# Optimization experiments

Measured on AMD Instinct MI355X. Metric: run time of the kernel, lower is better.

Reference implementation:

```python
import jax, jax.numpy as jnp
import numpy as np

NEG_SLOPE = 0.01  # torch F.leaky_relu default used in the DGL GAT-style layer


def grat_layer(h, src, dst, W, a, n_nodes):
    """One GRAT (GAT-style) layer.
    h: [N, d_in], src/dst: [E] int, W: [d_in, d_out], a: [2*d_out] (attn_fc weight
    on concat [z_src || z_dst]). Returns [N, d_out].
    """
    d_out = W.shape[1]
    z = h @ W                                   # [N, d_out]
    # attention logits per edge: a^T [z_src || z_dst]
    s_src = z @ a[:d_out]                       # [N]
    s_dst = z @ a[d_out:]                       # [N]
    e = jax.nn.leaky_relu(s_src[src] + s_dst[dst], NEG_SLOPE)  # [E]
    # numerically stable softmax over incoming edges of each dst node
    m = jax.ops.segment_max(e, dst, num_segments=n_nodes)      # [N]
    m = jnp.where(jnp.isfinite(m), m, 0.0)      # nodes with no in-edges
    w = jnp.exp(e - m[dst])                     # [E]
    denom = jax.ops.segment_sum(w, dst, num_segments=n_nodes)  # [N]
    alpha = w / jnp.maximum(denom, 1e-9)[dst]   # [E]
    # weighted scatter-aggregate of source features into dst
    out = jax.ops.segment_sum(alpha[:, None] * z[src], dst, num_segments=n_nodes)
    return out                                  # [N, d_out]


def setup_inputs() -> dict:
    key = jax.random.key(0)
    ks = jax.random.split(key, 10)
    N, E = 100000, 1600000
    IN, H1, H2, OUT = 128, 32, 32, 1
    feature = jax.random.normal(ks[0], (N, IN), dtype=jnp.float32)
    src = jax.random.randint(ks[1], (E,), 0, N, dtype=jnp.int32)
    dst = jax.random.randint(ks[2], (E,), 0, N, dtype=jnp.int32)
    s = 0.1
    W1 = jax.random.normal(ks[3], (IN, H1), dtype=jnp.float32) * s
    a1 = jax.random.normal(ks[4], (2 * H1,), dtype=jnp.float32) * s
    W2 = jax.random.normal(ks[5], (H1, H2), dtype=jnp.float32) * s
    a2 = jax.random.normal(ks[6], (2 * H2,), dtype=jnp.float32) * s
    W3 = jax.random.normal(ks[7], (H2, OUT), dtype=jnp.float32) * s
    a3 = jax.random.normal(ks[8], (2 * OUT,), dtype=jnp.float32) * s
    return {"feature": feature, "src": src, "dst": dst,
            "W1": W1, "a1": a1, "W2": W2, "a2": a2, "W3": W3, "a3": a3}


def reference(feature, src, dst, W1, a1, W2, a2, W3, a3):
    n = feature.shape[0]
    h = jax.nn.relu(grat_layer(feature, src, dst, W1, a1, n))
    h = jax.nn.relu(grat_layer(h, src, dst, W2, a2, n))
    h = grat_layer(h, src, dst, W3, a3, n)
    return jax.nn.sigmoid(h)                    # [N, 1]
```

## Files before the change

kernel.cpp:

```cpp
#include <hip/hip_runtime.h>
#include <cstdint>
#include <cstddef>

#define NEG_SLOPE 0.01f


__global__ __launch_bounds__(128) void gemm1_kernel(
    const float* __restrict__ h, const float* __restrict__ W,
    const float* __restrict__ a, float* __restrict__ z,
    float* __restrict__ s_src, float* __restrict__ s_dst, int N)
{
    __shared__ float Wl[128 * 32];
    int tid = threadIdx.x;
    int rowBase = blockIdx.x * 64;

    {
        const float4* W4 = (const float4*)W;
        float4* Wl4 = (float4*)Wl;
        for (int i = tid; i < 1024; i += 128) Wl4[i] = W4[i];
    }
    __syncthreads();

    int wv   = tid >> 6;
    int lane = tid & 63;
    int g    = lane >> 3;
    int l8   = lane & 7;
    int r0   = wv * 32 + g * 4;
    int col4 = l8 * 4;

    float acc[4][4];
#pragma unroll
    for (int i = 0; i < 4; i++)
#pragma unroll
        for (int c = 0; c < 4; c++) acc[i][c] = 0.f;

    const float4* h4  = (const float4*)h;
    const float4* Wl4 = (const float4*)Wl;

    size_t rowOff[4];
#pragma unroll
    for (int i = 0; i < 4; i++) {
        int r = rowBase + r0 + i;
        rowOff[i] = (size_t)((r < N) ? r : (N - 1)) * 32;
    }

#pragma unroll 2
    for (int kq = 0; kq < 32; kq++) {
        float4 w0 = Wl4[(kq * 4 + 0) * 8 + l8];
        float4 w1 = Wl4[(kq * 4 + 1) * 8 + l8];
        float4 w2 = Wl4[(kq * 4 + 2) * 8 + l8];
        float4 w3 = Wl4[(kq * 4 + 3) * 8 + l8];
#pragma unroll
        for (int i = 0; i < 4; i++) {
            float4 hv = h4[rowOff[i] + kq];
            acc[i][0] += hv.x * w0.x; acc[i][1] += hv.x * w0.y;
            acc[i][2] += hv.x * w0.z; acc[i][3] += hv.x * w0.w;
            acc[i][0] += hv.y * w1.x; acc[i][1] += hv.y * w1.y;
            acc[i][2] += hv.y * w1.z; acc[i][3] += hv.y * w1.w;
            acc[i][0] += hv.z * w2.x; acc[i][1] += hv.z * w2.y;
            acc[i][2] += hv.z * w2.z; acc[i][3] += hv.z * w2.w;
            acc[i][0] += hv.w * w3.x; acc[i][1] += hv.w * w3.y;
            acc[i][2] += hv.w * w3.z; acc[i][3] += hv.w * w3.w;
        }
    }

    float4 alo = ((const float4*)a)[l8];
    float4 ahi = ((const float4*)a)[8 + l8];
#pragma unroll
    for (int i = 0; i < 4; i++) {
        int row = rowBase + r0 + i;
        if (row < N) {
            float4 zv = make_float4(acc[i][0], acc[i][1], acc[i][2], acc[i][3]);
            *(float4*)&z[(size_t)row * 32 + col4] = zv;
            float ps = zv.x * alo.x + zv.y * alo.y + zv.z * alo.z + zv.w * alo.w;
            float pd = zv.x * ahi.x + zv.y * ahi.y + zv.z * ahi.z + zv.w * ahi.w;
            ps += __shfl_xor(ps, 1, 64); ps += __shfl_xor(ps, 2, 64); ps += __shfl_xor(ps, 4, 64);
            pd += __shfl_xor(pd, 1, 64); pd += __shfl_xor(pd, 2, 64); pd += __shfl_xor(pd, 4, 64);
            if (l8 == 0) { s_src[row] = ps; s_dst[row] = pd; }
        }
    }
}

__global__ __launch_bounds__(128) void gemm2_kernel(
    const float* __restrict__ h, const float* __restrict__ W,
    const float* __restrict__ a, float* __restrict__ z,
    float* __restrict__ s_src, float* __restrict__ s_dst, int N)
{
    __shared__ float Hl[64 * 44];
    __shared__ float Wl[32 * 32];
    int tid = threadIdx.x;
    int rowBase = blockIdx.x * 64;

    {
        const float4* W4 = (const float4*)W;
        float4* Wl4 = (float4*)Wl;
        for (int i = tid; i < 256; i += 128) Wl4[i] = W4[i];
    }
    {
        const float4* h4 = (const float4*)h;
        for (int i = tid; i < 64 * 8; i += 128) {
            int r = i >> 3, kq = i & 7;
            float4 v = (rowBase + r < N) ? h4[(size_t)(rowBase + r) * 8 + kq]
                                         : make_float4(0.f, 0.f, 0.f, 0.f);
            *(float4*)&Hl[r * 44 + kq * 4] = v;
        }
    }
    __syncthreads();

    int wv   = tid >> 6;
    int lane = tid & 63;
    int g    = lane >> 3;
    int l8   = lane & 7;
    int r0   = wv * 32 + g * 4;
    int col4 = l8 * 4;

    float acc[4][4];
#pragma unroll
    for (int i = 0; i < 4; i++)
#pragma unroll
        for (int c = 0; c < 4; c++) acc[i][c] = 0.f;

    const float4* H4  = (const float4*)Hl;
    const float4* Wl4 = (const float4*)Wl;

#pragma unroll
    for (int kq = 0; kq < 8; kq++) {
        float4 w0 = Wl4[(kq * 4 + 0) * 8 + l8];
        float4 w1 = Wl4[(kq * 4 + 1) * 8 + l8];
        float4 w2 = Wl4[(kq * 4 + 2) * 8 + l8];
        float4 w3 = Wl4[(kq * 4 + 3) * 8 + l8];
#pragma unroll
        for (int i = 0; i < 4; i++) {
            float4 hv = H4[(r0 + i) * 11 + kq];
            acc[i][0] += hv.x * w0.x; acc[i][1] += hv.x * w0.y;
            acc[i][2] += hv.x * w0.z; acc[i][3] += hv.x * w0.w;
            acc[i][0] += hv.y * w1.x; acc[i][1] += hv.y * w1.y;
            acc[i][2] += hv.y * w1.z; acc[i][3] += hv.y * w1.w;
            acc[i][0] += hv.z * w2.x; acc[i][1] += hv.z * w2.y;
            acc[i][2] += hv.z * w2.z; acc[i][3] += hv.z * w2.w;
            acc[i][0] += hv.w * w3.x; acc[i][1] += hv.w * w3.y;
            acc[i][2] += hv.w * w3.z; acc[i][3] += hv.w * w3.w;
        }
    }

    float4 alo = ((const float4*)a)[l8];
    float4 ahi = ((const float4*)a)[8 + l8];
#pragma unroll
    for (int i = 0; i < 4; i++) {
        int row = rowBase + r0 + i;
        if (row < N) {
            float4 zv = make_float4(acc[i][0], acc[i][1], acc[i][2], acc[i][3]);
            *(float4*)&z[(size_t)row * 32 + col4] = zv;
            float ps = zv.x * alo.x + zv.y * alo.y + zv.z * alo.z + zv.w * alo.w;
            float pd = zv.x * ahi.x + zv.y * ahi.y + zv.z * ahi.z + zv.w * ahi.w;
            ps += __shfl_xor(ps, 1, 64); ps += __shfl_xor(ps, 2, 64); ps += __shfl_xor(ps, 4, 64);
            pd += __shfl_xor(pd, 1, 64); pd += __shfl_xor(pd, 2, 64); pd += __shfl_xor(pd, 4, 64);
            if (l8 == 0) { s_src[row] = ps; s_dst[row] = pd; }
        }
    }
}

__global__ __launch_bounds__(256) void gemm3_kernel(
    const float* __restrict__ h, const float* __restrict__ W,
    const float* __restrict__ a, float2* __restrict__ zs,
    float* __restrict__ s_dst, int N)
{
    int i = blockIdx.x * 256 + threadIdx.x;
    if (i >= N) return;
    const float4* hp = (const float4*)(h + (size_t)i * 32);
    const float4* wp = (const float4*)W;
    float acc = 0.f;
#pragma unroll
    for (int c = 0; c < 8; c++) {
        float4 v = hp[c];
        float4 w = wp[c];
        acc += v.x * w.x + v.y * w.y + v.z * w.z + v.w * w.w;
    }
    zs[i] = make_float2(acc, acc * a[0]);
    s_dst[i] = acc * a[1];
}


#define TILE_E 4096
#define NB_MAX 512

__global__ __launch_bounds__(256) void csr_hist_kernel(
    const int* __restrict__ dst, int* __restrict__ counts,
    int E, int TB, int NB)
{
    __shared__ int hist[NB_MAX];
    int tid = threadIdx.x;
    int t = blockIdx.x;
    for (int b = tid; b < NB; b += 256) hist[b] = 0;
    __syncthreads();
    int base = t * TILE_E;
    for (int i = tid; i < TILE_E; i += 256) {
        int k = base + i;
        if (k < E) atomicAdd(&hist[dst[k] >> 8], 1);
    }
    __syncthreads();
    for (int b = tid; b < NB; b += 256) counts[b * TB + t] = hist[b];
}

__global__ __launch_bounds__(256) void scan1_kernel(
    const int* __restrict__ vals, int* __restrict__ incl,
    int* __restrict__ blockSums, int M)
{
    __shared__ int tmp[256];
    int tid = threadIdx.x;
    int i = blockIdx.x * 256 + tid;
    int v = (i < M) ? vals[i] : 0;
    tmp[tid] = v;
    __syncthreads();
#pragma unroll
    for (int off = 1; off < 256; off <<= 1) {
        int t = (tid >= off) ? tmp[tid - off] : 0;
        __syncthreads();
        tmp[tid] += t;
        __syncthreads();
    }
    if (i < M) incl[i] = tmp[tid];
    if (tid == 255) blockSums[blockIdx.x] = tmp[255];
}

__global__ __launch_bounds__(1024) void scan2_kernel(int* __restrict__ blockSums, int nb)
{
    __shared__ int tmp[1024];
    int tid = threadIdx.x;
    int v = (tid < nb) ? blockSums[tid] : 0;
    tmp[tid] = v;
    __syncthreads();
#pragma unroll
    for (int off = 1; off < 1024; off <<= 1) {
        int t = (tid >= off) ? tmp[tid - off] : 0;
        __syncthreads();
        tmp[tid] += t;
        __syncthreads();
    }
    if (tid < nb) blockSums[tid] = tmp[tid] - v;
}

__global__ __launch_bounds__(256) void scan3_kernel(
    const int* __restrict__ vals, const int* __restrict__ blockSums,
    int* __restrict__ cscan, int M, int E)
{
    int i = blockIdx.x * 256 + threadIdx.x;
    if (i < M) {
        cscan[i] = cscan[i] - vals[i] + blockSums[i >> 8];
    }
    if (i == 0) cscan[M] = E;
}

__global__ __launch_bounds__(256) void csr_scatter_kernel(
    const int* __restrict__ src, const int* __restrict__ dst,
    const int* __restrict__ cscan, int2* __restrict__ ebuf,
    int E, int TB, int NB)
{
    __shared__ int baseB[NB_MAX];
    __shared__ int cur[NB_MAX];
    int tid = threadIdx.x;
    int t = blockIdx.x;
    for (int b = tid; b < NB; b += 256) {
        baseB[b] = cscan[b * TB + t];
        cur[b] = 0;
    }
    __syncthreads();
    int base = t * TILE_E;
    for (int i = tid; i < TILE_E; i += 256) {
        int k = base + i;
        if (k < E) {
            int d = dst[k], s = src[k];
            int b = d >> 8;
            int r = atomicAdd(&cur[b], 1);
            ebuf[baseB[b] + r] = make_int2(s, d & 255);
        }
    }
}

__global__ __launch_bounds__(256) void csr_bucket_kernel(
    const int2* __restrict__ ebuf, const int* __restrict__ cscan,
    int* __restrict__ csr_src, int* __restrict__ offsets,
    int N, int E, int TB)
{
    __shared__ int2 eb[6144];
    __shared__ int hist[256];
    __shared__ int loff[256];
    __shared__ int tmp[256];
    int tid = threadIdx.x;
    int b = blockIdx.x;

    int beg = cscan[b * TB];
    int endv = cscan[(b + 1) * TB];
    int cnt = endv - beg;
    int first = b << 8;

    hist[tid] = 0;
    __syncthreads();

    bool inLds = (cnt <= 6144);
    for (int i = tid; i < cnt; i += 256) {
        int2 v = ebuf[beg + i];
        if (inLds) eb[i] = v;
        atomicAdd(&hist[v.y], 1);
    }
    __syncthreads();

    int hv = hist[tid];
    tmp[tid] = hv;
    __syncthreads();
#pragma unroll
    for (int off = 1; off < 256; off <<= 1) {
        int t = (tid >= off) ? tmp[tid - off] : 0;
        __syncthreads();
        tmp[tid] += t;
        __syncthreads();
    }
    loff[tid] = tmp[tid] - hv;
    __syncthreads();

    if (first + tid < N) offsets[first + tid] = beg + loff[tid];
    if (b == 0 && tid == 0) offsets[N] = E;

    hist[tid] = 0;
    __syncthreads();

    for (int i = tid; i < cnt; i += 256) {
        int2 v = inLds ? eb[i] : ebuf[beg + i];
        int r = atomicAdd(&hist[v.y], 1);
        csr_src[beg + loff[v.y] + r] = v.x;
    }
}


__global__ __launch_bounds__(256) void agg32_fused_kernel(
    const int* __restrict__ offsets, const int* __restrict__ csr_src,
    const float* __restrict__ s_src, const float* __restrict__ s_dst,
    const float* __restrict__ z, float* __restrict__ h, int N)
{
    __shared__ float2 wsbuf[8 * 128];
    int g    = threadIdx.x >> 5;
    int lane = threadIdx.x & 31;
    int node = blockIdx.x * 8 + g;
    if (node >= N) return;
    float2* ws = &wsbuf[g * 128];

    int beg = offsets[node], end = offsets[node + 1];
    int deg = end - beg;
    float sd = s_dst[node];
    float o = 0.f;
    float rden;

    if (deg <= 128) {
        int   sreg[4];
        float ev[4];
        int nIter = (deg + 31) >> 5;
        float m = -3.0e38f;
#pragma unroll 4
        for (int it = 0; it < nIter; ++it) {
            int p = beg + it * 32 + lane;
            float e = -3.0e38f;
            int s = 0;
            if (p < end) {
                s = csr_src[p];
                e = s_src[s] + sd;
                e = (e > 0.f) ? e : NEG_SLOPE * e;
            }
            sreg[it] = s;
            ev[it] = e;
            m = fmaxf(m, e);
        }
#pragma unroll
        for (int off = 16; off > 0; off >>= 1) m = fmaxf(m, __shfl_xor(m, off, 32));

        float l = 0.f;
#pragma unroll 4
        for (int it = 0; it < nIter; ++it) {
            int p = beg + it * 32 + lane;
            float w = (p < end) ? __expf(ev[it] - m) : 0.f;
            ws[it * 32 + lane] = make_float2(w, __int_as_float(sreg[it]));
            l += w;
        }
#pragma unroll
        for (int off = 16; off > 0; off >>= 1) l += __shfl_xor(l, off, 32);
        rden = 1.f / fmaxf(l, 1e-9f);

        int p = 0;
        for (; p + 4 <= deg; p += 4) {
            float2 a0 = ws[p],     a1 = ws[p + 1];
            float2 a2 = ws[p + 2], a3 = ws[p + 3];
            int s0 = __float_as_int(a0.y), s1 = __float_as_int(a1.y);
            int s2 = __float_as_int(a2.y), s3 = __float_as_int(a3.y);
            float z0 = z[(size_t)s0 * 32 + lane];
            float z1 = z[(size_t)s1 * 32 + lane];
            float z2 = z[(size_t)s2 * 32 + lane];
            float z3 = z[(size_t)s3 * 32 + lane];
            o += a0.x * z0;
            o += a1.x * z1;
            o += a2.x * z2;
            o += a3.x * z3;
        }
        for (; p < deg; ++p) {
            float2 aa = ws[p];
            o += aa.x * z[(size_t)__float_as_int(aa.y) * 32 + lane];
        }
    } else {
        float m = -3.0e38f;
        for (int p = beg + lane; p < end; p += 32) {
            float e = s_src[csr_src[p]] + sd;
            e = (e > 0.f) ? e : NEG_SLOPE * e;
            m = fmaxf(m, e);
        }
#pragma unroll
        for (int off = 16; off > 0; off >>= 1) m = fmaxf(m, __shfl_xor(m, off, 32));
        float l = 0.f;
        for (int p = beg + lane; p < end; p += 32) {
            float e = s_src[csr_src[p]] + sd;
            e = (e > 0.f) ? e : NEG_SLOPE * e;
            l += __expf(e - m);
        }
#pragma unroll
        for (int off = 16; off > 0; off >>= 1) l += __shfl_xor(l, off, 32);
        rden = 1.f / fmaxf(l, 1e-9f);
        for (int p = beg; p < end; ++p) {
            int s = csr_src[p];
            float e = s_src[s] + sd;
            e = (e > 0.f) ? e : NEG_SLOPE * e;
            float w = __expf(e - m);
            o += w * z[(size_t)s * 32 + lane];
        }
    }

    float v = o * rden;
    h[(size_t)node * 32 + lane] = (v > 0.f) ? v : 0.f;
}

__global__ __launch_bounds__(256) void agg1_fused_kernel(
    const int* __restrict__ offsets, const int* __restrict__ csr_src,
    const float2* __restrict__ zs, const float* __restrict__ s_dst,
    float* __restrict__ out, int N)
{
    int node = blockIdx.x * 8 + (threadIdx.x >> 5);
    int lane = threadIdx.x & 31;
    if (node >= N) return;

    int beg = offsets[node], end = offsets[node + 1];
    int deg = end - beg;
    float sd = s_dst[node];

    if (deg <= 128) {
        float ev[4], zv[4];
        int nIter = (deg + 31) >> 5;
        float m = -3.0e38f;
#pragma unroll 4
        for (int it = 0; it < nIter; ++it) {
            int p = beg + it * 32 + lane;
            float e = -3.0e38f, zz = 0.f;
            if (p < end) {
                float2 v2 = zs[csr_src[p]];
                zz = v2.x;
                e = v2.y + sd;
                e = (e > 0.f) ? e : NEG_SLOPE * e;
            }
            ev[it] = e; zv[it] = zz;
            m = fmaxf(m, e);
        }
#pragma unroll
        for (int off = 16; off > 0; off >>= 1) m = fmaxf(m, __shfl_xor(m, off, 32));
        float l = 0.f, o = 0.f;
#pragma unroll 4
        for (int it = 0; it < nIter; ++it) {
            int p = beg + it * 32 + lane;
            float w = (p < end) ? __expf(ev[it] - m) : 0.f;
            l += w;
            o += w * zv[it];
        }
#pragma unroll
        for (int off = 16; off > 0; off >>= 1) {
            l += __shfl_xor(l, off, 32);
            o += __shfl_xor(o, off, 32);
        }
        if (lane == 0) {
            float v = o / fmaxf(l, 1e-9f);
            out[node] = 1.f / (1.f + __expf(-v));
        }
    } else {
        float m = -3.0e38f;
        for (int p = beg + lane; p < end; p += 32) {
            float e = zs[csr_src[p]].y + sd;
            e = (e > 0.f) ? e : NEG_SLOPE * e;
            m = fmaxf(m, e);
        }
#pragma unroll
        for (int off = 16; off > 0; off >>= 1) m = fmaxf(m, __shfl_xor(m, off, 32));
        float l = 0.f, o = 0.f;
        for (int p = beg + lane; p < end; p += 32) {
            float2 v2 = zs[csr_src[p]];
            float e = v2.y + sd;
            e = (e > 0.f) ? e : NEG_SLOPE * e;
            float w = __expf(e - m);
            l += w; o += w * v2.x;
        }
#pragma unroll
        for (int off = 16; off > 0; off >>= 1) {
            l += __shfl_xor(l, off, 32);
            o += __shfl_xor(o, off, 32);
        }
        if (lane == 0) {
            float v = o / fmaxf(l, 1e-9f);
            out[node] = 1.f / (1.f + __expf(-v));
        }
    }
}


extern "C" void kernel_launch(void* const* d_in, const int* in_sizes, int n_in,
                              void* d_out, int out_size, void* d_ws, size_t ws_size,
                              hipStream_t stream)
{
    const float* feature = (const float*)d_in[0];
    const int*   src     = (const int*)d_in[1];
    const int*   dst     = (const int*)d_in[2];
    const float* W1      = (const float*)d_in[3];
    const float* a1      = (const float*)d_in[4];
    const float* W2      = (const float*)d_in[5];
    const float* a2      = (const float*)d_in[6];
    const float* W3      = (const float*)d_in[7];
    const float* a3      = (const float*)d_in[8];
    float* out = (float*)d_out;

    const int N = in_sizes[0] / 128;
    const int E = in_sizes[1];

    const int TB = (E + TILE_E - 1) / TILE_E;
    const int NB = (N + 255) >> 8;
    const int M  = NB * TB;

    char* p = (char*)d_ws;
    float* zbuf    = (float*)p;  p += (size_t)N * 32 * sizeof(float);
    float* hbuf    = (float*)p;  p += (size_t)N * 32 * sizeof(float);
    float* s_src   = (float*)p;  p += (size_t)N * sizeof(float);
    float* s_dst   = (float*)p;  p += (size_t)N * sizeof(float);
    int*   offsets = (int*)p;    p += ((size_t)N + 1) * sizeof(int);
    int*   counts  = (int*)p;    p += ((size_t)M + 1) * sizeof(int);
    int*   cscan   = (int*)p;    p += ((size_t)M + 1) * sizeof(int);
    int*   blockSums = (int*)p;  p += 1024 * sizeof(int);
    int2*  ebuf    = (int2*)p;   p += (size_t)E * sizeof(int2);
    int*   csr_src = (int*)p;    p += (size_t)E * sizeof(int);

    const int nodeBlocks8  = (N + 7) / 8;
    const int nodeBlocks   = (N + 255) / 256;
    const int gemmBlocks64 = (N + 63) / 64;
    const int scanBlocksM  = (M + 255) / 256;

    hipLaunchKernelGGL(csr_hist_kernel, dim3(TB), dim3(256), 0, stream,
                       dst, counts, E, TB, NB);
    hipLaunchKernelGGL(scan1_kernel, dim3(scanBlocksM), dim3(256), 0, stream,
                       counts, cscan, blockSums, M);
    hipLaunchKernelGGL(scan2_kernel, dim3(1), dim3(1024), 0, stream,
                       blockSums, scanBlocksM);
    hipLaunchKernelGGL(scan3_kernel, dim3(scanBlocksM), dim3(256), 0, stream,
                       counts, blockSums, cscan, M, E);
    hipLaunchKernelGGL(csr_scatter_kernel, dim3(TB), dim3(256), 0, stream,
                       src, dst, cscan, ebuf, E, TB, NB);
    hipLaunchKernelGGL(csr_bucket_kernel, dim3(NB), dim3(256), 0, stream,
                       ebuf, cscan, csr_src, offsets, N, E, TB);

    hipLaunchKernelGGL(gemm1_kernel, dim3(gemmBlocks64), dim3(128), 0, stream,
                       feature, W1, a1, zbuf, s_src, s_dst, N);
    hipLaunchKernelGGL(agg32_fused_kernel, dim3(nodeBlocks8), dim3(256), 0, stream,
                       offsets, csr_src, s_src, s_dst, zbuf, hbuf, N);

    hipLaunchKernelGGL(gemm2_kernel, dim3(gemmBlocks64), dim3(128), 0, stream,
                       hbuf, W2, a2, zbuf, s_src, s_dst, N);
    hipLaunchKernelGGL(agg32_fused_kernel, dim3(nodeBlocks8), dim3(256), 0, stream,
                       offsets, csr_src, s_src, s_dst, zbuf, hbuf, N);

    float2* zs = (float2*)zbuf;
    hipLaunchKernelGGL(gemm3_kernel, dim3(nodeBlocks), dim3(256), 0, stream,
                       hbuf, W3, a3, zs, s_dst, N);
    hipLaunchKernelGGL(agg1_fused_kernel, dim3(nodeBlocks8), dim3(256), 0, stream,
                       offsets, csr_src, zs, s_dst, out, N);
}
```

Before: 280.7 us.

## Store intermediate features in bf16 and pack CSR edge buffer into single ints

The two hidden-layer GEMMs now write z as bf16 instead of fp32, and the aggregation kernels gather and convert bf16 rows. This halves the bytes of the random per-edge feature gathers. Attention scores are still computed from the fp32 accumulators. Separately, the CSR build packs source and local destination into one 32-bit int, which halves the edge buffer traffic and lets more buckets fit in LDS. Risks are precision loss in the aggregated features and the packing only being valid for source ids below 2^23.

```diff
diff --git a/kernel.cpp b/kernel.cpp
--- a/kernel.cpp
+++ b/kernel.cpp
@@ -1,13 +1,23 @@
 #include <hip/hip_runtime.h>
+#include <hip/hip_bf16.h>
 #include <cstdint>
 #include <cstddef>
 
 #define NEG_SLOPE 0.01f
 
+static __device__ __forceinline__ unsigned short f2bf(float f) {
+    __hip_bfloat16 b = __float2bfloat16(f);
+    return *(unsigned short*)&b;
+}
+static __device__ __forceinline__ float bf2f(unsigned short u) {
+    __hip_bfloat16 b = *(__hip_bfloat16*)&u;
+    return __bfloat162float(b);
+}
+
 
 __global__ __launch_bounds__(128) void gemm1_kernel(
     const float* __restrict__ h, const float* __restrict__ W,
-    const float* __restrict__ a, float* __restrict__ z,
+    const float* __restrict__ a, unsigned short* __restrict__ zb,
     float* __restrict__ s_src, float* __restrict__ s_dst, int N)
 {
     __shared__ float Wl[128 * 32];
@@ -70,10 +80,11 @@
     for (int i = 0; i < 4; i++) {
         int row = rowBase + r0 + i;
         if (row < N) {
-            float4 zv = make_float4(acc[i][0], acc[i][1], acc[i][2], acc[i][3]);
-            *(float4*)&z[(size_t)row * 32 + col4] = zv;
-            float ps = zv.x * alo.x + zv.y * alo.y + zv.z * alo.z + zv.w * alo.w;
-            float pd = zv.x * ahi.x + zv.y * ahi.y + zv.z * ahi.z + zv.w * ahi.w;
+            ushort4 zv4 = make_ushort4(f2bf(acc[i][0]), f2bf(acc[i][1]),
+                                       f2bf(acc[i][2]), f2bf(acc[i][3]));
+            *(ushort4*)&zb[(size_t)row * 32 + col4] = zv4;
+            float ps = acc[i][0] * alo.x + acc[i][1] * alo.y + acc[i][2] * alo.z + acc[i][3] * alo.w;
+            float pd = acc[i][0] * ahi.x + acc[i][1] * ahi.y + acc[i][2] * ahi.z + acc[i][3] * ahi.w;
             ps += __shfl_xor(ps, 1, 64); ps += __shfl_xor(ps, 2, 64); ps += __shfl_xor(ps, 4, 64);
             pd += __shfl_xor(pd, 1, 64); pd += __shfl_xor(pd, 2, 64); pd += __shfl_xor(pd, 4, 64);
             if (l8 == 0) { s_src[row] = ps; s_dst[row] = pd; }
@@ -83,7 +94,7 @@
 
 __global__ __launch_bounds__(128) void gemm2_kernel(
     const float* __restrict__ h, const float* __restrict__ W,
-    const float* __restrict__ a, float* __restrict__ z,
+    const float* __restrict__ a, unsigned short* __restrict__ zb,
     float* __restrict__ s_src, float* __restrict__ s_dst, int N)
 {
     __shared__ float Hl[64 * 44];
@@ -149,10 +160,11 @@
     for (int i = 0; i < 4; i++) {
         int row = rowBase + r0 + i;
         if (row < N) {
-            float4 zv = make_float4(acc[i][0], acc[i][1], acc[i][2], acc[i][3]);
-            *(float4*)&z[(size_t)row * 32 + col4] = zv;
-            float ps = zv.x * alo.x + zv.y * alo.y + zv.z * alo.z + zv.w * alo.w;
-            float pd = zv.x * ahi.x + zv.y * ahi.y + zv.z * ahi.z + zv.w * ahi.w;
+            ushort4 zv4 = make_ushort4(f2bf(acc[i][0]), f2bf(acc[i][1]),
+                                       f2bf(acc[i][2]), f2bf(acc[i][3]));
+            *(ushort4*)&zb[(size_t)row * 32 + col4] = zv4;
+            float ps = acc[i][0] * alo.x + acc[i][1] * alo.y + acc[i][2] * alo.z + acc[i][3] * alo.w;
+            float pd = acc[i][0] * ahi.x + acc[i][1] * ahi.y + acc[i][2] * ahi.z + acc[i][3] * ahi.w;
             ps += __shfl_xor(ps, 1, 64); ps += __shfl_xor(ps, 2, 64); ps += __shfl_xor(ps, 4, 64);
             pd += __shfl_xor(pd, 1, 64); pd += __shfl_xor(pd, 2, 64); pd += __shfl_xor(pd, 4, 64);
             if (l8 == 0) { s_src[row] = ps; s_dst[row] = pd; }
@@ -253,7 +265,7 @@
 
 __global__ __launch_bounds__(256) void csr_scatter_kernel(
     const int* __restrict__ src, const int* __restrict__ dst,
-    const int* __restrict__ cscan, int2* __restrict__ ebuf,
+    const int* __restrict__ cscan, int* __restrict__ ebuf,
     int E, int TB, int NB)
 {
     __shared__ int baseB[NB_MAX];
@@ -272,17 +284,17 @@
             int d = dst[k], s = src[k];
             int b = d >> 8;
             int r = atomicAdd(&cur[b], 1);
-            ebuf[baseB[b] + r] = make_int2(s, d & 255);
+            ebuf[baseB[b] + r] = (s << 8) | (d & 255);
         }
     }
 }
 
 __global__ __launch_bounds__(256) void csr_bucket_kernel(
-    const int2* __restrict__ ebuf, const int* __restrict__ cscan,
+    const int* __restrict__ ebuf, const int* __restrict__ cscan,
     int* __restrict__ csr_src, int* __restrict__ offsets,
     int N, int E, int TB)
 {
-    __shared__ int2 eb[6144];
+    __shared__ int eb[8192];
     __shared__ int hist[256];
     __shared__ int loff[256];
     __shared__ int tmp[256];
@@ -297,11 +309,11 @@
     hist[tid] = 0;
     __syncthreads();
 
-    bool inLds = (cnt <= 6144);
+    bool inLds = (cnt <= 8192);
     for (int i = tid; i < cnt; i += 256) {
-        int2 v = ebuf[beg + i];
+        int v = ebuf[beg + i];
         if (inLds) eb[i] = v;
-        atomicAdd(&hist[v.y], 1);
+        atomicAdd(&hist[v & 255], 1);
     }
     __syncthreads();
 
@@ -325,9 +337,10 @@
     __syncthreads();
 
     for (int i = tid; i < cnt; i += 256) {
-        int2 v = inLds ? eb[i] : ebuf[beg + i];
-        int r = atomicAdd(&hist[v.y], 1);
-        csr_src[beg + loff[v.y] + r] = v.x;
+        int v = inLds ? eb[i] : ebuf[beg + i];
+        int d8 = v & 255;
+        int r = atomicAdd(&hist[d8], 1);
+        csr_src[beg + loff[d8] + r] = v >> 8;
     }
 }
 
@@ -335,7 +348,7 @@
 __global__ __launch_bounds__(256) void agg32_fused_kernel(
     const int* __restrict__ offsets, const int* __restrict__ csr_src,
     const float* __restrict__ s_src, const float* __restrict__ s_dst,
-    const float* __restrict__ z, float* __restrict__ h, int N)
+    const unsigned short* __restrict__ zb, float* __restrict__ h, int N)
 {
     __shared__ float2 wsbuf[8 * 128];
     int g    = threadIdx.x >> 5;
@@ -390,18 +403,18 @@
             float2 a2 = ws[p + 2], a3 = ws[p + 3];
             int s0 = __float_as_int(a0.y), s1 = __float_as_int(a1.y);
             int s2 = __float_as_int(a2.y), s3 = __float_as_int(a3.y);
-            float z0 = z[(size_t)s0 * 32 + lane];
-            float z1 = z[(size_t)s1 * 32 + lane];
-            float z2 = z[(size_t)s2 * 32 + lane];
-            float z3 = z[(size_t)s3 * 32 + lane];
-            o += a0.x * z0;
-            o += a1.x * z1;
-            o += a2.x * z2;
-            o += a3.x * z3;
+            unsigned short u0 = zb[(size_t)s0 * 32 + lane];
+            unsigned short u1 = zb[(size_t)s1 * 32 + lane];
+            unsigned short u2 = zb[(size_t)s2 * 32 + lane];
+            unsigned short u3 = zb[(size_t)s3 * 32 + lane];
+            o += a0.x * bf2f(u0);
+            o += a1.x * bf2f(u1);
+            o += a2.x * bf2f(u2);
+            o += a3.x * bf2f(u3);
         }
         for (; p < deg; ++p) {
             float2 aa = ws[p];
-            o += aa.x * z[(size_t)__float_as_int(aa.y) * 32 + lane];
+            o += aa.x * bf2f(zb[(size_t)__float_as_int(aa.y) * 32 + lane]);
         }
     } else {
         float m = -3.0e38f;
@@ -426,7 +439,7 @@
             float e = s_src[s] + sd;
             e = (e > 0.f) ? e : NEG_SLOPE * e;
             float w = __expf(e - m);
-            o += w * z[(size_t)s * 32 + lane];
+            o += w * bf2f(zb[(size_t)s * 32 + lane]);
         }
     }
 
@@ -536,15 +549,16 @@
     const int M  = NB * TB;
 
     char* p = (char*)d_ws;
-    float* zbuf    = (float*)p;  p += (size_t)N * 32 * sizeof(float);
+    unsigned short* zb = (unsigned short*)p;  p += (size_t)N * 32 * sizeof(unsigned short);
     float* hbuf    = (float*)p;  p += (size_t)N * 32 * sizeof(float);
+    float* zs32    = (float*)p;  p += (size_t)N * 2 * sizeof(float);
     float* s_src   = (float*)p;  p += (size_t)N * sizeof(float);
     float* s_dst   = (float*)p;  p += (size_t)N * sizeof(float);
     int*   offsets = (int*)p;    p += ((size_t)N + 1) * sizeof(int);
     int*   counts  = (int*)p;    p += ((size_t)M + 1) * sizeof(int);
     int*   cscan   = (int*)p;    p += ((size_t)M + 1) * sizeof(int);
     int*   blockSums = (int*)p;  p += 1024 * sizeof(int);
-    int2*  ebuf    = (int2*)p;   p += (size_t)E * sizeof(int2);
+    int*   ebuf    = (int*)p;    p += (size_t)E * sizeof(int);
     int*   csr_src = (int*)p;    p += (size_t)E * sizeof(int);
 
     const int nodeBlocks8  = (N + 7) / 8;
@@ -566,16 +580,16 @@
                        ebuf, cscan, csr_src, offsets, N, E, TB);
 
     hipLaunchKernelGGL(gemm1_kernel, dim3(gemmBlocks64), dim3(128), 0, stream,
-                       feature, W1, a1, zbuf, s_src, s_dst, N);
+                       feature, W1, a1, zb, s_src, s_dst, N);
     hipLaunchKernelGGL(agg32_fused_kernel, dim3(nodeBlocks8), dim3(256), 0, stream,
-                       offsets, csr_src, s_src, s_dst, zbuf, hbuf, N);
+                       offsets, csr_src, s_src, s_dst, zb, hbuf, N);
 
     hipLaunchKernelGGL(gemm2_kernel, dim3(gemmBlocks64), dim3(128), 0, stream,
-                       hbuf, W2, a2, zbuf, s_src, s_dst, N);
+                       hbuf, W2, a2, zb, s_src, s_dst, N);
     hipLaunchKernelGGL(agg32_fused_kernel, dim3(nodeBlocks8), dim3(256), 0, stream,
-                       offsets, csr_src, s_src, s_dst, zbuf, hbuf, N);
-
-    float2* zs = (float2*)zbuf;
+                       offsets, csr_src, s_src, s_dst, zb, hbuf, N);
+
+    float2* zs = (float2*)zs32;
     hipLaunchKernelGGL(gemm3_kernel, dim3(nodeBlocks), dim3(256), 0, stream,
                        hbuf, W3, a3, zs, s_dst, N);
     hipLaunchKernelGGL(agg1_fused_kernel, dim3(nodeBlocks8), dim3(256), 0, stream,
```

Result: no change. 276.8 us (-1.4%).
